# Optimization experiments

Hardware: AMD Instinct MI355X
Metric: run time of the kernel (lower is better)

Reference implementation:

```python
import jax, jax.numpy as jnp
import numpy as np

N_NODES = 10000


def _gcn_norm(edge_index, n):
    # PyG GCNConv default: add self-loops, symmetric deg^{-1/2} normalization
    src, dst = edge_index[0], edge_index[1]
    loop = jnp.arange(n, dtype=edge_index.dtype)
    src = jnp.concatenate([src, loop])
    dst = jnp.concatenate([dst, loop])
    deg = jax.ops.segment_sum(jnp.ones_like(dst, dtype=jnp.float32), dst, num_segments=n)
    inv_sqrt = jnp.where(deg > 0, jax.lax.rsqrt(jnp.maximum(deg, 1e-12)), 0.0)
    norm = inv_sqrt[src] * inv_sqrt[dst]  # [E + N]
    return src, dst, norm


def _gcn_conv(x, W, b, src, dst, norm, n):
    h = x @ W                              # [N, out]
    msg = h[src] * norm[:, None]           # gather + scale  [E+N, out]
    out = jax.ops.segment_sum(msg, dst, num_segments=n)  # scatter-add
    return out + b


def setup_inputs() -> dict:
    key = jax.random.key(0)
    ks = jax.random.split(key, 8)
    n, e = N_NODES, 640000
    cin, ch, cout = 128, 128, 64

    def glorot(k, fan_in, fan_out):
        s = float(np.sqrt(6.0 / (fan_in + fan_out)))
        return jax.random.uniform(k, (fan_in, fan_out), jnp.float32, -s, s)

    return {
        "x": jax.random.normal(ks[0], (n, cin), jnp.float32),
        "edge_index": jax.random.randint(ks[1], (2, e), 0, n, jnp.int64),
        "W1": glorot(ks[2], cin, ch),
        "b1": jnp.zeros((ch,), jnp.float32),
        "W2": glorot(ks[3], ch, ch),
        "b2": jnp.zeros((ch,), jnp.float32),
        "W3": glorot(ks[4], ch, cout),
        "b3": jnp.zeros((cout,), jnp.float32),
    }


def reference(x, edge_index, W1, b1, W2, b2, W3, b3):
    n = x.shape[0]
    src, dst, norm = _gcn_norm(edge_index, n)
    h = jax.nn.relu(_gcn_conv(x, W1, b1, src, dst, norm, n))
    h = jax.nn.relu(_gcn_conv(h, W2, b2, src, dst, norm, n))
    return _gcn_conv(h, W3, b3, src, dst, norm, n)
```

## Files before the change

### kernel.cpp

```cpp
#include <hip/hip_runtime.h>

#define NN 10000
#define NE 640000
#define NB 313
#define RSTRIDE 2688
#define EPB 2048
#define G1B 1250

__device__ __forceinline__ unsigned short f2bf(float x) {
    unsigned u = __float_as_uint(x);
    u += 0x7FFFu + ((u >> 16) & 1u);
    return (unsigned short)(u >> 16);
}
__device__ __forceinline__ float bflo(unsigned u) { return __uint_as_float(u << 16); }
__device__ __forceinline__ float bfhi(unsigned u) { return __uint_as_float(u & 0xFFFF0000u); }

struct SMpart { int hist[NB]; int scanv[NB + 1]; int gbase[NB]; int lcur[NB];
                unsigned stage[EPB]; };
struct SMbuild { int sbase[NB + 1]; int hist32[32]; int cur32[32];
                 unsigned stage[RSTRIDE]; };
union SMu {
    SMpart p;
    SMbuild b;
    float xs[16][128];
};

__global__ void zero_kernel(int* __restrict__ cur) {
    if (threadIdx.x < NB) cur[threadIdx.x] = 0;
}

__device__ __forceinline__ void gemm1_block(const float* __restrict__ X,
                                            const float* __restrict__ W,
                                            unsigned short* __restrict__ Y,
                                            float (*xs)[128], int vb, int tid) {
    int row0 = vb * 8;
    for (int idx = tid; idx < 8 * 128; idx += 256) {
        int r = idx >> 7, k = idx & 127;
        xs[r][k] = X[(size_t)(row0 + r) * 128 + k];
    }
    __syncthreads();
    int ct = tid & 31, r = tid >> 5, c = ct * 4;
    float4 acc = make_float4(0.f, 0.f, 0.f, 0.f);
    #pragma unroll 8
    for (int k = 0; k < 128; ++k) {
        float xv = xs[r][k];
        float4 w = *reinterpret_cast<const float4*>(W + (size_t)k * 128 + c);
        acc.x += xv * w.x; acc.y += xv * w.y; acc.z += xv * w.z; acc.w += xv * w.w;
    }
    ushort4 o;
    o.x = f2bf(acc.x); o.y = f2bf(acc.y); o.z = f2bf(acc.z); o.w = f2bf(acc.w);
    *reinterpret_cast<ushort4*>(Y + (size_t)(row0 + r) * 128 + c) = o;
}

template<int NOUTc, int ROWS>
__device__ __forceinline__ void gemm_bf_block(const unsigned short* __restrict__ Xb,
                                              const float* __restrict__ W,
                                              unsigned short* __restrict__ Y,
                                              float (*xs)[128], int vb, int tid) {
    int row0 = vb * ROWS;
    const unsigned* Xu = reinterpret_cast<const unsigned*>(Xb + (size_t)row0 * 128);
    for (int idx = tid; idx < ROWS * 64; idx += 256) {
        unsigned u = Xu[idx];
        int r = idx >> 6, kk = idx & 63;
        xs[r][kk * 2]     = bflo(u);
        xs[r][kk * 2 + 1] = bfhi(u);
    }
    __syncthreads();
    constexpr int COLT = NOUTc / 4;
    int ct = tid % COLT, r = tid / COLT, c = ct * 4;
    float4 acc = make_float4(0.f, 0.f, 0.f, 0.f);
    #pragma unroll 8
    for (int k = 0; k < 128; ++k) {
        float xv = xs[r][k];
        float4 w = *reinterpret_cast<const float4*>(W + (size_t)k * NOUTc + c);
        acc.x += xv * w.x; acc.y += xv * w.y; acc.z += xv * w.z; acc.w += xv * w.w;
    }
    ushort4 o;
    o.x = f2bf(acc.x); o.y = f2bf(acc.y); o.z = f2bf(acc.z); o.w = f2bf(acc.w);
    *reinterpret_cast<ushort4*>(Y + (size_t)(row0 + r) * NOUTc + c) = o;
}

__device__ __forceinline__ void partition_block(const int* __restrict__ src,
                                                const int* __restrict__ dst,
                                                int* __restrict__ bcur,
                                                unsigned* __restrict__ edge_part,
                                                SMpart& p, int bid, int tid) {
    for (int i = tid; i < NB; i += 256) p.hist[i] = 0;
    __syncthreads();
    int gi = bid * EPB + tid * 8;
    unsigned rec[8];
    bool act = gi < NE;
    if (act) {
        int4 s0 = *reinterpret_cast<const int4*>(src + gi);
        int4 s1 = *reinterpret_cast<const int4*>(src + gi + 4);
        int4 d0 = *reinterpret_cast<const int4*>(dst + gi);
        int4 d1 = *reinterpret_cast<const int4*>(dst + gi + 4);
        rec[0] = ((unsigned)d0.x << 14) | (unsigned)s0.x;
        rec[1] = ((unsigned)d0.y << 14) | (unsigned)s0.y;
        rec[2] = ((unsigned)d0.z << 14) | (unsigned)s0.z;
        rec[3] = ((unsigned)d0.w << 14) | (unsigned)s0.w;
        rec[4] = ((unsigned)d1.x << 14) | (unsigned)s1.x;
        rec[5] = ((unsigned)d1.y << 14) | (unsigned)s1.y;
        rec[6] = ((unsigned)d1.z << 14) | (unsigned)s1.z;
        rec[7] = ((unsigned)d1.w << 14) | (unsigned)s1.w;
        #pragma unroll
        for (int k = 0; k < 8; ++k) atomicAdd(&p.hist[rec[k] >> 19], 1);
    }
    __syncthreads();
    if (tid < 64) {
        int carry = 0;
        for (int c = 0; c < NB; c += 64) {
            int idx = c + tid;
            int v = (idx < NB) ? p.hist[idx] : 0;
            int incl = v;
            #pragma unroll
            for (int d = 1; d < 64; d <<= 1) {
                int t = __shfl_up(incl, d, 64);
                if (tid >= d) incl += t;
            }
            if (idx < NB) p.scanv[idx] = carry + incl - v;
            carry += __shfl(incl, 63, 64);
        }
        if (tid == 0) p.scanv[NB] = carry;
    }
    __syncthreads();
    for (int bb = tid; bb < NB; bb += 256) {
        p.gbase[bb] = atomicAdd(&bcur[bb], p.hist[bb]);
        p.lcur[bb]  = p.scanv[bb];
    }
    __syncthreads();
    if (act) {
        #pragma unroll
        for (int k = 0; k < 8; ++k) {
            int bb = rec[k] >> 19;
            int pp = atomicAdd(&p.lcur[bb], 1);
            p.stage[pp] = rec[k];
        }
    }
    __syncthreads();
    int tot = p.scanv[NB];
    for (int i = tid; i < tot; i += 256) {
        unsigned r = p.stage[i];
        int bb = r >> 19;
        edge_part[bb * RSTRIDE + p.gbase[bb] + (i - p.scanv[bb])] = r;
    }
}

__device__ __forceinline__ void build_block(const unsigned* __restrict__ edge_part,
                                            const int* __restrict__ bcur,
                                            int* __restrict__ offs,
                                            float* __restrict__ inv_sqrt,
                                            unsigned short* __restrict__ edge_src,
                                            SMbuild& b, int bid, int tid) {
    if (tid < 64) {
        int carry = 0;
        for (int c = 0; c < NB; c += 64) {
            int idx = c + tid;
            int v = (idx < NB) ? bcur[idx] : 0;
            int incl = v;
            #pragma unroll
            for (int d = 1; d < 64; d <<= 1) {
                int t = __shfl_up(incl, d, 64);
                if (tid >= d) incl += t;
            }
            if (idx < NB) b.sbase[idx] = carry + incl - v;
            carry += __shfl(incl, 63, 64);
        }
    }
    if (tid < 32) b.hist32[tid] = 0;
    __syncthreads();
    int cnt = bcur[bid];
    int base = b.sbase[bid];
    const unsigned* part = edge_part + (size_t)bid * RSTRIDE;
    for (int k = tid; k < cnt; k += 256)
        atomicAdd(&b.hist32[(part[k] >> 14) & 31], 1);
    __syncthreads();
    if (tid < 32) {
        int v = b.hist32[tid];
        int incl = v;
        #pragma unroll
        for (int d = 1; d < 32; d <<= 1) {
            int t = __shfl_up(incl, d, 32);
            if (tid >= d) incl += t;
        }
        int excl = incl - v;
        b.cur32[tid] = excl;
        int node = bid * 32 + tid;
        if (node < NN) {
            offs[node] = base + excl;
            inv_sqrt[node] = rsqrtf((float)(v + 1));
        }
        if (bid == NB - 1 && tid == 0) offs[NN] = base + cnt;
    }
    __syncthreads();
    for (int k = tid; k < cnt; k += 256) {
        unsigned r = part[k];
        int pp = atomicAdd(&b.cur32[(r >> 14) & 31], 1);
        b.stage[pp] = r & 0x3FFFu;
    }
    __syncthreads();
    for (int k = tid; k < cnt; k += 256)
        edge_src[base + k] = (unsigned short)b.stage[k];
}

__global__ __launch_bounds__(256) void part_gemm1_kernel(
        const int* __restrict__ src, const int* __restrict__ dst,
        int* __restrict__ bcur, unsigned* __restrict__ edge_part,
        const float* __restrict__ X, const float* __restrict__ W,
        unsigned short* __restrict__ Y) {
    __shared__ SMu sm;
    int tid = threadIdx.x;
    if (blockIdx.x >= NB) {
        gemm1_block(X, W, Y, sm.xs, blockIdx.x - NB, tid);
        return;
    }
    partition_block(src, dst, bcur, edge_part, sm.p, blockIdx.x, tid);
}

__global__ __launch_bounds__(256) void build_kernel(
        const unsigned* __restrict__ edge_part, const int* __restrict__ bcur,
        int* __restrict__ offs, float* __restrict__ inv_sqrt,
        unsigned short* __restrict__ edge_src) {
    __shared__ SMu sm;
    build_block(edge_part, bcur, offs, inv_sqrt, edge_src, sm.b,
                blockIdx.x, threadIdx.x);
}

__global__ __launch_bounds__(128) void agg128_kernel(
        const unsigned short* __restrict__ H, const unsigned short* __restrict__ esrc,
        const int* __restrict__ offs, const float* __restrict__ isqv,
        const float* __restrict__ bias, unsigned* __restrict__ Aout) {
    __shared__ float4 red[32];
    int node = blockIdx.x;
    int tid = threadIdx.x, lane = tid & 63, wv = tid >> 6;
    int l = lane & 31, g = lane >> 5;
    int s = offs[node], e = offs[node + 1];
    int deg = e - s;
    int half = ((deg >> 1) + 7) & ~7;
    int js = s + wv * half;
    if (js > e) js = e;
    int mid = s + half;
    int je = wv ? e : (mid < e ? mid : e);
    int colb = l * 4;
    float4 acc = make_float4(0.f, 0.f, 0.f, 0.f);
    int j = js;
    for (; j + 8 <= je; j += 8) {
        int sA = esrc[j + g],     sB = esrc[j + 2 + g];
        int sC = esrc[j + 4 + g], sD = esrc[j + 6 + g];
        float wA = isqv[sA], wB = isqv[sB], wC = isqv[sC], wD = isqv[sD];
        uint2 a = *reinterpret_cast<const uint2*>(H + (size_t)sA * 128 + colb);
        uint2 b = *reinterpret_cast<const uint2*>(H + (size_t)sB * 128 + colb);
        uint2 c = *reinterpret_cast<const uint2*>(H + (size_t)sC * 128 + colb);
        uint2 d = *reinterpret_cast<const uint2*>(H + (size_t)sD * 128 + colb);
        acc.x += wA * bflo(a.x); acc.y += wA * bfhi(a.x);
        acc.z += wA * bflo(a.y); acc.w += wA * bfhi(a.y);
        acc.x += wB * bflo(b.x); acc.y += wB * bfhi(b.x);
        acc.z += wB * bflo(b.y); acc.w += wB * bfhi(b.y);
        acc.x += wC * bflo(c.x); acc.y += wC * bfhi(c.x);
        acc.z += wC * bflo(c.y); acc.w += wC * bfhi(c.y);
        acc.x += wD * bflo(d.x); acc.y += wD * bfhi(d.x);
        acc.z += wD * bflo(d.y); acc.w += wD * bfhi(d.y);
    }
    for (; j + 2 <= je; j += 2) {
        int sA = esrc[j + g];
        float wA = isqv[sA];
        uint2 a = *reinterpret_cast<const uint2*>(H + (size_t)sA * 128 + colb);
        acc.x += wA * bflo(a.x); acc.y += wA * bfhi(a.x);
        acc.z += wA * bflo(a.y); acc.w += wA * bfhi(a.y);
    }
    if (j < je && g == 0) {
        int sA = esrc[j];
        float wA = isqv[sA];
        uint2 a = *reinterpret_cast<const uint2*>(H + (size_t)sA * 128 + colb);
        acc.x += wA * bflo(a.x); acc.y += wA * bfhi(a.x);
        acc.z += wA * bflo(a.y); acc.w += wA * bfhi(a.y);
    }
    acc.x += __shfl_down(acc.x, 32);
    acc.y += __shfl_down(acc.y, 32);
    acc.z += __shfl_down(acc.z, 32);
    acc.w += __shfl_down(acc.w, 32);
    if (wv == 1 && lane < 32) red[lane] = acc;
    __syncthreads();
    if (wv == 0 && lane < 32) {
        float4 r = red[lane];
        acc.x += r.x; acc.y += r.y; acc.z += r.z; acc.w += r.w;
        float isq = isqv[node];
        uint2 uv = *reinterpret_cast<const uint2*>(H + (size_t)node * 128 + colb);
        float self = isq * isq;
        float o0 = fmaxf(acc.x * isq + self * bflo(uv.x) + bias[colb],     0.f);
        float o1 = fmaxf(acc.y * isq + self * bfhi(uv.x) + bias[colb + 1], 0.f);
        float o2 = fmaxf(acc.z * isq + self * bflo(uv.y) + bias[colb + 2], 0.f);
        float o3 = fmaxf(acc.w * isq + self * bfhi(uv.y) + bias[colb + 3], 0.f);
        uint2 ov;
        ov.x = (unsigned)f2bf(o0) | ((unsigned)f2bf(o1) << 16);
        ov.y = (unsigned)f2bf(o2) | ((unsigned)f2bf(o3) << 16);
        *reinterpret_cast<uint2*>(Aout + (size_t)node * 64 + l * 2) = ov;
    }
}

__global__ __launch_bounds__(128) void agg64_kernel(
        const unsigned short* __restrict__ H, const unsigned short* __restrict__ esrc,
        const int* __restrict__ offs, const float* __restrict__ isqv,
        const float* __restrict__ bias, float* __restrict__ out) {
    __shared__ float2 red[32];
    int node = blockIdx.x;
    int tid = threadIdx.x, lane = tid & 63, wv = tid >> 6;
    int l = lane & 31, g = lane >> 5;
    int s = offs[node], e = offs[node + 1];
    int deg = e - s;
    int half = ((deg >> 1) + 7) & ~7;
    int js = s + wv * half;
    if (js > e) js = e;
    int mid = s + half;
    int je = wv ? e : (mid < e ? mid : e);
    int colb = l * 2;
    float2 acc = make_float2(0.f, 0.f);
    int j = js;
    for (; j + 8 <= je; j += 8) {
        int sA = esrc[j + g],     sB = esrc[j + 2 + g];
        int sC = esrc[j + 4 + g], sD = esrc[j + 6 + g];
        float wA = isqv[sA], wB = isqv[sB], wC = isqv[sC], wD = isqv[sD];
        unsigned a = *reinterpret_cast<const unsigned*>(H + (size_t)sA * 64 + colb);
        unsigned b = *reinterpret_cast<const unsigned*>(H + (size_t)sB * 64 + colb);
        unsigned c = *reinterpret_cast<const unsigned*>(H + (size_t)sC * 64 + colb);
        unsigned d = *reinterpret_cast<const unsigned*>(H + (size_t)sD * 64 + colb);
        acc.x += wA * bflo(a); acc.y += wA * bfhi(a);
        acc.x += wB * bflo(b); acc.y += wB * bfhi(b);
        acc.x += wC * bflo(c); acc.y += wC * bfhi(c);
        acc.x += wD * bflo(d); acc.y += wD * bfhi(d);
    }
    for (; j + 2 <= je; j += 2) {
        int sA = esrc[j + g];
        float wA = isqv[sA];
        unsigned a = *reinterpret_cast<const unsigned*>(H + (size_t)sA * 64 + colb);
        acc.x += wA * bflo(a); acc.y += wA * bfhi(a);
    }
    if (j < je && g == 0) {
        int sA = esrc[j];
        float wA = isqv[sA];
        unsigned a = *reinterpret_cast<const unsigned*>(H + (size_t)sA * 64 + colb);
        acc.x += wA * bflo(a); acc.y += wA * bfhi(a);
    }
    acc.x += __shfl_down(acc.x, 32);
    acc.y += __shfl_down(acc.y, 32);
    if (wv == 1 && lane < 32) red[lane] = acc;
    __syncthreads();
    if (wv == 0 && lane < 32) {
        float2 r = red[lane];
        acc.x += r.x; acc.y += r.y;
        float isq = isqv[node];
        unsigned uv = *reinterpret_cast<const unsigned*>(H + (size_t)node * 64 + colb);
        float self = isq * isq;
        float2 ov;
        ov.x = acc.x * isq + self * bflo(uv) + bias[colb];
        ov.y = acc.y * isq + self * bfhi(uv) + bias[colb + 1];
        *reinterpret_cast<float2*>(out + (size_t)node * 64 + colb) = ov;
    }
}

template<int N>
__global__ __launch_bounds__(256) void gemm_bf_kernel(
        const unsigned short* __restrict__ X, const float* __restrict__ W,
        unsigned short* __restrict__ Y) {
    __shared__ SMu sm;
    gemm_bf_block<N, 256 / (N / 4)>(X, W, Y, sm.xs, blockIdx.x, threadIdx.x);
}

extern "C" void kernel_launch(void* const* d_in, const int* in_sizes, int n_in,
                              void* d_out, int out_size, void* d_ws, size_t ws_size,
                              hipStream_t stream) {
    const float* x  = (const float*)d_in[0];
    const int*   ei = (const int*)d_in[1];
    const float* W1 = (const float*)d_in[2];
    const float* b1 = (const float*)d_in[3];
    const float* W2 = (const float*)d_in[4];
    const float* b2 = (const float*)d_in[5];
    const float* W3 = (const float*)d_in[6];
    const float* b3 = (const float*)d_in[7];
    float* out = (float*)d_out;

    const int* src = ei;
    const int* dst = ei + NE;

    char* ws = (char*)d_ws;
    int*            bcur      = (int*)(ws);
    float*          inv_sqrt  = (float*)(ws + 4096);
    int*            offs      = (int*)(ws + 45056);
    unsigned*       edge_part = (unsigned*)(ws + 86016);
    unsigned short* edge_src  = (unsigned short*)(ws + 3451392);
    unsigned short* T1        = (unsigned short*)(ws + 6011392);
    unsigned short* A         = (unsigned short*)(ws + 8571392);
    unsigned short* T2        = (unsigned short*)edge_part;
    unsigned short* T3        = T1;

    zero_kernel<<<1, 320, 0, stream>>>(bcur);
    part_gemm1_kernel<<<NB + G1B, 256, 0, stream>>>(src, dst, bcur, edge_part,
                                                    x, W1, T1);
    build_kernel<<<NB, 256, 0, stream>>>(edge_part, bcur, offs, inv_sqrt, edge_src);
    agg128_kernel<<<NN, 128, 0, stream>>>(T1, edge_src, offs, inv_sqrt, b1,
                                          (unsigned*)A);
    gemm_bf_kernel<128><<<NN / 8, 256, 0, stream>>>(A, W2, T2);
    agg128_kernel<<<NN, 128, 0, stream>>>(T2, edge_src, offs, inv_sqrt, b2,
                                          (unsigned*)A);
    gemm_bf_kernel<64><<<NN / 16, 256, 0, stream>>>(A, W3, T3);
    agg64_kernel<<<NN, 128, 0, stream>>>(T3, edge_src, offs, inv_sqrt, b3, out);
}
```

Baseline: 133.2 us.

## Prescale GEMM outputs by inv_sqrt and widen per-lane gather to 16 bytes

The second and third GEMMs now multiply each output row by the source node's inverse sqrt degree. The following aggregation can then sum neighbour rows without loading a per-edge weight. The aggregation kernels are also reshaped so each lane loads 8 (or 4) bf16 values with 16-byte (or 8-byte) loads, and 4 edge groups are processed per wave instead of 2, with a two-step shuffle reduction. This removes the per-edge isqv gather and halves the number of load instructions per edge. The cost is an extra bf16 rounding of the scaled values and more register pressure.

```diff
diff --git a/kernel.cpp b/kernel.cpp
--- a/kernel.cpp
+++ b/kernel.cpp
@@ -14,6 +14,23 @@
 }
 __device__ __forceinline__ float bflo(unsigned u) { return __uint_as_float(u << 16); }
 __device__ __forceinline__ float bfhi(unsigned u) { return __uint_as_float(u & 0xFFFF0000u); }
+
+__device__ __forceinline__ void acc8w(float* acc, uint4 u, float w) {
+    acc[0] += w * bflo(u.x); acc[1] += w * bfhi(u.x);
+    acc[2] += w * bflo(u.y); acc[3] += w * bfhi(u.y);
+    acc[4] += w * bflo(u.z); acc[5] += w * bfhi(u.z);
+    acc[6] += w * bflo(u.w); acc[7] += w * bfhi(u.w);
+}
+__device__ __forceinline__ void acc8p(float* acc, uint4 u) {
+    acc[0] += bflo(u.x); acc[1] += bfhi(u.x);
+    acc[2] += bflo(u.y); acc[3] += bfhi(u.y);
+    acc[4] += bflo(u.z); acc[5] += bfhi(u.z);
+    acc[6] += bflo(u.w); acc[7] += bfhi(u.w);
+}
+__device__ __forceinline__ void acc4p(float* acc, uint2 u) {
+    acc[0] += bflo(u.x); acc[1] += bfhi(u.x);
+    acc[2] += bflo(u.y); acc[3] += bfhi(u.y);
+}
 
 struct SMpart { int hist[NB]; int scanv[NB + 1]; int gbase[NB]; int lcur[NB];
                 unsigned stage[EPB]; };
@@ -52,9 +69,10 @@
     *reinterpret_cast<ushort4*>(Y + (size_t)(row0 + r) * 128 + c) = o;
 }
 
-template<int NOUTc, int ROWS>
+template<int NOUTc, int ROWS, bool SCALE>
 __device__ __forceinline__ void gemm_bf_block(const unsigned short* __restrict__ Xb,
                                               const float* __restrict__ W,
+                                              const float* __restrict__ isqv,
                                               unsigned short* __restrict__ Y,
                                               float (*xs)[128], int vb, int tid) {
     int row0 = vb * ROWS;
@@ -75,9 +93,14 @@
         float4 w = *reinterpret_cast<const float4*>(W + (size_t)k * NOUTc + c);
         acc.x += xv * w.x; acc.y += xv * w.y; acc.z += xv * w.z; acc.w += xv * w.w;
     }
+    int gr = row0 + r;
+    if (SCALE) {
+        float sc = isqv[gr];
+        acc.x *= sc; acc.y *= sc; acc.z *= sc; acc.w *= sc;
+    }
     ushort4 o;
     o.x = f2bf(acc.x); o.y = f2bf(acc.y); o.z = f2bf(acc.z); o.w = f2bf(acc.w);
-    *reinterpret_cast<ushort4*>(Y + (size_t)(row0 + r) * NOUTc + c) = o;
+    *reinterpret_cast<ushort4*>(Y + (size_t)gr * NOUTc + c) = o;
 }
 
 __device__ __forceinline__ void partition_block(const int* __restrict__ src,
@@ -226,144 +249,155 @@
                 blockIdx.x, threadIdx.x);
 }
 
+template<bool PS>
 __global__ __launch_bounds__(128) void agg128_kernel(
         const unsigned short* __restrict__ H, const unsigned short* __restrict__ esrc,
         const int* __restrict__ offs, const float* __restrict__ isqv,
-        const float* __restrict__ bias, unsigned* __restrict__ Aout) {
-    __shared__ float4 red[32];
+        const float* __restrict__ bias, uint4* __restrict__ Aout) {
+    __shared__ float red[16][9];
     int node = blockIdx.x;
     int tid = threadIdx.x, lane = tid & 63, wv = tid >> 6;
-    int l = lane & 31, g = lane >> 5;
+    int l = lane & 15, g = lane >> 4;
     int s = offs[node], e = offs[node + 1];
     int deg = e - s;
-    int half = ((deg >> 1) + 7) & ~7;
+    int half = ((deg >> 1) + 3) & ~3;
+    int js = s + wv * half;
+    if (js > e) js = e;
+    int mid = s + half;
+    int je = wv ? e : (mid < e ? mid : e);
+    int colb = l * 8;
+    float acc[8];
+    #pragma unroll
+    for (int i = 0; i < 8; ++i) acc[i] = 0.f;
+    int j = js;
+    for (; j + 16 <= je; j += 16) {
+        int sA = esrc[j + g],      sB = esrc[j + 4 + g];
+        int sC = esrc[j + 8 + g],  sD = esrc[j + 12 + g];
+        uint4 a = *reinterpret_cast<const uint4*>(H + (size_t)sA * 128 + colb);
+        uint4 b = *reinterpret_cast<const uint4*>(H + (size_t)sB * 128 + colb);
+        uint4 c = *reinterpret_cast<const uint4*>(H + (size_t)sC * 128 + colb);
+        uint4 d = *reinterpret_cast<const uint4*>(H + (size_t)sD * 128 + colb);
+        if (PS) {
+            acc8p(acc, a); acc8p(acc, b); acc8p(acc, c); acc8p(acc, d);
+        } else {
+            float wA = isqv[sA], wB = isqv[sB], wC = isqv[sC], wD = isqv[sD];
+            acc8w(acc, a, wA); acc8w(acc, b, wB);
+            acc8w(acc, c, wC); acc8w(acc, d, wD);
+        }
+    }
+    for (; j + 4 <= je; j += 4) {
+        int sA = esrc[j + g];
+        uint4 a = *reinterpret_cast<const uint4*>(H + (size_t)sA * 128 + colb);
+        if (PS) { acc8p(acc, a); }
+        else    { acc8w(acc, a, isqv[sA]); }
+    }
+    int rem = je - j;
+    if (g < rem) {
+        int sA = esrc[j + g];
+        uint4 a = *reinterpret_cast<const uint4*>(H + (size_t)sA * 128 + colb);
+        if (PS) { acc8p(acc, a); }
+        else    { acc8w(acc, a, isqv[sA]); }
+    }
+    #pragma unroll
+    for (int i = 0; i < 8; ++i) {
+        acc[i] += __shfl_down(acc[i], 32);
+        acc[i] += __shfl_down(acc[i], 16);
+    }
+    if (wv == 1 && lane < 16) {
+        #pragma unroll
+        for (int i = 0; i < 8; ++i) red[l][i] = acc[i];
+    }
+    __syncthreads();
+    if (wv == 0 && lane < 16) {
+        float isq = isqv[node];
+        uint4 uv = *reinterpret_cast<const uint4*>(H + (size_t)node * 128 + colb);
+        float sv[8] = { bflo(uv.x), bfhi(uv.x), bflo(uv.y), bfhi(uv.y),
+                        bflo(uv.z), bfhi(uv.z), bflo(uv.w), bfhi(uv.w) };
+        float o[8];
+        #pragma unroll
+        for (int i = 0; i < 8; ++i) {
+            float a = acc[i] + red[l][i];
+            a += PS ? sv[i] : isq * sv[i];
+            o[i] = fmaxf(isq * a + bias[colb + i], 0.f);
+        }
+        uint4 ov;
+        ov.x = (unsigned)f2bf(o[0]) | ((unsigned)f2bf(o[1]) << 16);
+        ov.y = (unsigned)f2bf(o[2]) | ((unsigned)f2bf(o[3]) << 16);
+        ov.z = (unsigned)f2bf(o[4]) | ((unsigned)f2bf(o[5]) << 16);
+        ov.w = (unsigned)f2bf(o[6]) | ((unsigned)f2bf(o[7]) << 16);
+        Aout[(size_t)node * 16 + l] = ov;
+    }
+}
+
+__global__ __launch_bounds__(128) void agg64_kernel(
+        const unsigned short* __restrict__ H, const unsigned short* __restrict__ esrc,
+        const int* __restrict__ offs, const float* __restrict__ isqv,
+        const float* __restrict__ bias, float* __restrict__ out) {
+    __shared__ float red[16][5];
+    int node = blockIdx.x;
+    int tid = threadIdx.x, lane = tid & 63, wv = tid >> 6;
+    int l = lane & 15, g = lane >> 4;
+    int s = offs[node], e = offs[node + 1];
+    int deg = e - s;
+    int half = ((deg >> 1) + 3) & ~3;
     int js = s + wv * half;
     if (js > e) js = e;
     int mid = s + half;
     int je = wv ? e : (mid < e ? mid : e);
     int colb = l * 4;
-    float4 acc = make_float4(0.f, 0.f, 0.f, 0.f);
+    float acc[4] = {0.f, 0.f, 0.f, 0.f};
     int j = js;
-    for (; j + 8 <= je; j += 8) {
-        int sA = esrc[j + g],     sB = esrc[j + 2 + g];
-        int sC = esrc[j + 4 + g], sD = esrc[j + 6 + g];
-        float wA = isqv[sA], wB = isqv[sB], wC = isqv[sC], wD = isqv[sD];
-        uint2 a = *reinterpret_cast<const uint2*>(H + (size_t)sA * 128 + colb);
-        uint2 b = *reinterpret_cast<const uint2*>(H + (size_t)sB * 128 + colb);
-        uint2 c = *reinterpret_cast<const uint2*>(H + (size_t)sC * 128 + colb);
-        uint2 d = *reinterpret_cast<const uint2*>(H + (size_t)sD * 128 + colb);
-        acc.x += wA * bflo(a.x); acc.y += wA * bfhi(a.x);
-        acc.z += wA * bflo(a.y); acc.w += wA * bfhi(a.y);
-        acc.x += wB * bflo(b.x); acc.y += wB * bfhi(b.x);
-        acc.z += wB * bflo(b.y); acc.w += wB * bfhi(b.y);
-        acc.x += wC * bflo(c.x); acc.y += wC * bfhi(c.x);
-        acc.z += wC * bflo(c.y); acc.w += wC * bfhi(c.y);
-        acc.x += wD * bflo(d.x); acc.y += wD * bfhi(d.x);
-        acc.z += wD * bflo(d.y); acc.w += wD * bfhi(d.y);
-    }
-    for (; j + 2 <= je; j += 2) {
+    for (; j + 16 <= je; j += 16) {
+        int sA = esrc[j + g],      sB = esrc[j + 4 + g];
+        int sC = esrc[j + 8 + g],  sD = esrc[j + 12 + g];
+        uint2 a = *reinterpret_cast<const uint2*>(H + (size_t)sA * 64 + colb);
+        uint2 b = *reinterpret_cast<const uint2*>(H + (size_t)sB * 64 + colb);
+        uint2 c = *reinterpret_cast<const uint2*>(H + (size_t)sC * 64 + colb);
+        uint2 d = *reinterpret_cast<const uint2*>(H + (size_t)sD * 64 + colb);
+        acc4p(acc, a); acc4p(acc, b); acc4p(acc, c); acc4p(acc, d);
+    }
+    for (; j + 4 <= je; j += 4) {
         int sA = esrc[j + g];
-        float wA = isqv[sA];
-        uint2 a = *reinterpret_cast<const uint2*>(H + (size_t)sA * 128 + colb);
-        acc.x += wA * bflo(a.x); acc.y += wA * bfhi(a.x);
-        acc.z += wA * bflo(a.y); acc.w += wA * bfhi(a.y);
-    }
-    if (j < je && g == 0) {
-        int sA = esrc[j];
-        float wA = isqv[sA];
-        uint2 a = *reinterpret_cast<const uint2*>(H + (size_t)sA * 128 + colb);
-        acc.x += wA * bflo(a.x); acc.y += wA * bfhi(a.x);
-        acc.z += wA * bflo(a.y); acc.w += wA * bfhi(a.y);
-    }
-    acc.x += __shfl_down(acc.x, 32);
-    acc.y += __shfl_down(acc.y, 32);
-    acc.z += __shfl_down(acc.z, 32);
-    acc.w += __shfl_down(acc.w, 32);
-    if (wv == 1 && lane < 32) red[lane] = acc;
-    __syncthreads();
-    if (wv == 0 && lane < 32) {
-        float4 r = red[lane];
-        acc.x += r.x; acc.y += r.y; acc.z += r.z; acc.w += r.w;
+        uint2 a = *reinterpret_cast<const uint2*>(H + (size_t)sA * 64 + colb);
+        acc4p(acc, a);
+    }
+    int rem = je - j;
+    if (g < rem) {
+        int sA = esrc[j + g];
+        uint2 a = *reinterpret_cast<const uint2*>(H + (size_t)sA * 64 + colb);
+        acc4p(acc, a);
+    }
+    #pragma unroll
+    for (int i = 0; i < 4; ++i) {
+        acc[i] += __shfl_down(acc[i], 32);
+        acc[i] += __shfl_down(acc[i], 16);
+    }
+    if (wv == 1 && lane < 16) {
+        #pragma unroll
+        for (int i = 0; i < 4; ++i) red[l][i] = acc[i];
+    }
+    __syncthreads();
+    if (wv == 0 && lane < 16) {
         float isq = isqv[node];
-        uint2 uv = *reinterpret_cast<const uint2*>(H + (size_t)node * 128 + colb);
-        float self = isq * isq;
-        float o0 = fmaxf(acc.x * isq + self * bflo(uv.x) + bias[colb],     0.f);
-        float o1 = fmaxf(acc.y * isq + self * bfhi(uv.x) + bias[colb + 1], 0.f);
-        float o2 = fmaxf(acc.z * isq + self * bflo(uv.y) + bias[colb + 2], 0.f);
-        float o3 = fmaxf(acc.w * isq + self * bfhi(uv.y) + bias[colb + 3], 0.f);
-        uint2 ov;
-        ov.x = (unsigned)f2bf(o0) | ((unsigned)f2bf(o1) << 16);
-        ov.y = (unsigned)f2bf(o2) | ((unsigned)f2bf(o3) << 16);
-        *reinterpret_cast<uint2*>(Aout + (size_t)node * 64 + l * 2) = ov;
-    }
-}
-
-__global__ __launch_bounds__(128) void agg64_kernel(
-        const unsigned short* __restrict__ H, const unsigned short* __restrict__ esrc,
-        const int* __restrict__ offs, const float* __restrict__ isqv,
-        const float* __restrict__ bias, float* __restrict__ out) {
-    __shared__ float2 red[32];
-    int node = blockIdx.x;
-    int tid = threadIdx.x, lane = tid & 63, wv = tid >> 6;
-    int l = lane & 31, g = lane >> 5;
-    int s = offs[node], e = offs[node + 1];
-    int deg = e - s;
-    int half = ((deg >> 1) + 7) & ~7;
-    int js = s + wv * half;
-    if (js > e) js = e;
-    int mid = s + half;
-    int je = wv ? e : (mid < e ? mid : e);
-    int colb = l * 2;
-    float2 acc = make_float2(0.f, 0.f);
-    int j = js;
-    for (; j + 8 <= je; j += 8) {
-        int sA = esrc[j + g],     sB = esrc[j + 2 + g];
-        int sC = esrc[j + 4 + g], sD = esrc[j + 6 + g];
-        float wA = isqv[sA], wB = isqv[sB], wC = isqv[sC], wD = isqv[sD];
-        unsigned a = *reinterpret_cast<const unsigned*>(H + (size_t)sA * 64 + colb);
-        unsigned b = *reinterpret_cast<const unsigned*>(H + (size_t)sB * 64 + colb);
-        unsigned c = *reinterpret_cast<const unsigned*>(H + (size_t)sC * 64 + colb);
-        unsigned d = *reinterpret_cast<const unsigned*>(H + (size_t)sD * 64 + colb);
-        acc.x += wA * bflo(a); acc.y += wA * bfhi(a);
-        acc.x += wB * bflo(b); acc.y += wB * bfhi(b);
-        acc.x += wC * bflo(c); acc.y += wC * bfhi(c);
-        acc.x += wD * bflo(d); acc.y += wD * bfhi(d);
-    }
-    for (; j + 2 <= je; j += 2) {
-        int sA = esrc[j + g];
-        float wA = isqv[sA];
-        unsigned a = *reinterpret_cast<const unsigned*>(H + (size_t)sA * 64 + colb);
-        acc.x += wA * bflo(a); acc.y += wA * bfhi(a);
-    }
-    if (j < je && g == 0) {
-        int sA = esrc[j];
-        float wA = isqv[sA];
-        unsigned a = *reinterpret_cast<const unsigned*>(H + (size_t)sA * 64 + colb);
-        acc.x += wA * bflo(a); acc.y += wA * bfhi(a);
-    }
-    acc.x += __shfl_down(acc.x, 32);
-    acc.y += __shfl_down(acc.y, 32);
-    if (wv == 1 && lane < 32) red[lane] = acc;
-    __syncthreads();
-    if (wv == 0 && lane < 32) {
-        float2 r = red[lane];
-        acc.x += r.x; acc.y += r.y;
-        float isq = isqv[node];
-        unsigned uv = *reinterpret_cast<const unsigned*>(H + (size_t)node * 64 + colb);
-        float self = isq * isq;
-        float2 ov;
-        ov.x = acc.x * isq + self * bflo(uv) + bias[colb];
-        ov.y = acc.y * isq + self * bfhi(uv) + bias[colb + 1];
-        *reinterpret_cast<float2*>(out + (size_t)node * 64 + colb) = ov;
-    }
-}
-
-template<int N>
+        uint2 uv = *reinterpret_cast<const uint2*>(H + (size_t)node * 64 + colb);
+        float sv[4] = { bflo(uv.x), bfhi(uv.x), bflo(uv.y), bfhi(uv.y) };
+        float4 ov;
+        float o[4];
+        #pragma unroll
+        for (int i = 0; i < 4; ++i)
+            o[i] = isq * (acc[i] + red[l][i] + sv[i]) + bias[colb + i];
+        ov.x = o[0]; ov.y = o[1]; ov.z = o[2]; ov.w = o[3];
+        *reinterpret_cast<float4*>(out + (size_t)node * 64 + colb) = ov;
+    }
+}
+
+template<int N, bool SCALE>
 __global__ __launch_bounds__(256) void gemm_bf_kernel(
         const unsigned short* __restrict__ X, const float* __restrict__ W,
-        unsigned short* __restrict__ Y) {
+        const float* __restrict__ isqv, unsigned short* __restrict__ Y) {
     __shared__ SMu sm;
-    gemm_bf_block<N, 256 / (N / 4)>(X, W, Y, sm.xs, blockIdx.x, threadIdx.x);
+    gemm_bf_block<N, 256 / (N / 4), SCALE>(X, W, isqv, Y, sm.xs,
+                                           blockIdx.x, threadIdx.x);
 }
 
 extern "C" void kernel_launch(void* const* d_in, const int* in_sizes, int n_in,
@@ -397,11 +431,11 @@
     part_gemm1_kernel<<<NB + G1B, 256, 0, stream>>>(src, dst, bcur, edge_part,
                                                     x, W1, T1);
     build_kernel<<<NB, 256, 0, stream>>>(edge_part, bcur, offs, inv_sqrt, edge_src);
-    agg128_kernel<<<NN, 128, 0, stream>>>(T1, edge_src, offs, inv_sqrt, b1,
-                                          (unsigned*)A);
-    gemm_bf_kernel<128><<<NN / 8, 256, 0, stream>>>(A, W2, T2);
-    agg128_kernel<<<NN, 128, 0, stream>>>(T2, edge_src, offs, inv_sqrt, b2,
-                                          (unsigned*)A);
-    gemm_bf_kernel<64><<<NN / 16, 256, 0, stream>>>(A, W3, T3);
+    agg128_kernel<false><<<NN, 128, 0, stream>>>(T1, edge_src, offs, inv_sqrt, b1,
+                                                 (uint4*)A);
+    gemm_bf_kernel<128, true><<<NN / 8, 256, 0, stream>>>(A, W2, inv_sqrt, T2);
+    agg128_kernel<true><<<NN, 128, 0, stream>>>(T2, edge_src, offs, inv_sqrt, b2,
+                                                (uint4*)A);
+    gemm_bf_kernel<64, true><<<NN / 16, 256, 0, stream>>>(A, W3, inv_sqrt, T3);
     agg64_kernel<<<NN, 128, 0, stream>>>(T3, edge_src, offs, inv_sqrt, b3, out);
 }
```

Measured after the change: 121.4 us. 1.1x faster.
